# Optimization experiments

Measured on AMD Instinct MI355X. Metric: run time of the kernel, lower is better.

## Reference

```python
import jax, jax.numpy as jnp
import numpy as np

RADIUS = 0.2
NSAMPLE = 32
USE_XYZ = True


def setup_inputs() -> dict:
    key = jax.random.key(0)
    k1, k2, k3 = jax.random.split(key, 3)
    B, N, NP, C = 16, 4096, 1024, 64
    xyz = jax.random.uniform(k1, (B, N, 3), dtype=jnp.float32)
    new_xyz = jax.random.uniform(k2, (B, NP, 3), dtype=jnp.float32)
    points = jax.random.normal(k3, (B, C, N), dtype=jnp.float32)
    return {"xyz": xyz, "new_xyz": new_xyz, "points": points}


def ball_query(radius, nsample, xyz, new_xyz):
    """Replicates the CUDA ball_query: for each center, the first `nsample`
    points (in index order) with squared distance < radius^2. Unfilled slots
    are set to the first in-radius index (0 if none in radius)."""
    B, N, _ = xyz.shape
    NP = new_xyz.shape[1]
    # [B, NP, N] squared distances
    d2 = jnp.sum((new_xyz[:, :, None, :] - xyz[:, None, :, :]) ** 2, axis=-1)
    mask = d2 < (radius * radius)
    order = jnp.cumsum(mask.astype(jnp.int32), axis=-1)  # 1-based rank among in-radius pts
    cnt = order[..., -1]                                  # [B, NP] in-radius count
    # slot for each point: rank-1 if it is one of the first nsample in-radius, else dummy
    slot = jnp.where(mask & (order <= nsample), order - 1, nsample)
    bb = jnp.arange(B, dtype=jnp.int32)[:, None, None]
    pp = jnp.arange(NP, dtype=jnp.int32)[None, :, None]
    nn = jnp.broadcast_to(jnp.arange(N, dtype=jnp.int32)[None, None, :], (B, NP, N))
    idx = jnp.zeros((B, NP, nsample + 1), dtype=jnp.int32).at[bb, pp, slot].set(nn)
    idx = idx[..., :nsample]
    # replicate first in-radius index into unfilled slots (stays 0 if cnt == 0)
    filled = jnp.arange(nsample)[None, None, :] < jnp.minimum(cnt, nsample)[..., None]
    idx = jnp.where(filled, idx, idx[..., :1])
    return idx


def reference(xyz, new_xyz, points):
    idx = ball_query(RADIUS, NSAMPLE, xyz, new_xyz)          # [B, NP, NS] int32
    # gather xyz: [B, NP, NS, 3] -> [B, 3, NP, NS]
    grouped_xyz = jax.vmap(lambda x, i: x[i])(xyz, idx)
    grouped_xyz = jnp.transpose(grouped_xyz, (0, 3, 1, 2))
    # centroid subtract
    grouped_xyz = grouped_xyz - jnp.transpose(new_xyz, (0, 2, 1))[..., None]
    # gather features: points [B, C, N] -> [B, C, NP, NS]
    grouped_points = jax.vmap(lambda p, i: p[:, i])(points, idx)
    if USE_XYZ:
        new_points = jnp.concatenate([grouped_xyz, grouped_points], axis=1)
    else:
        new_points = grouped_points
    return new_points
```

## Files before the change

### kernel.cpp

```cpp
#include <hip/hip_runtime.h>
#include <hip/hip_bf16.h>

constexpr int B  = 16;
constexpr int N  = 4096;
constexpr int NP = 1024;
constexpr int C  = 64;
constexpr int NS = 32;
constexpr int OC = C + 3;
constexpr float R2 = 0.2f * 0.2f;

typedef float v4f __attribute__((ext_vector_type(4)));
typedef int   v4i __attribute__((ext_vector_type(4)));

__global__ __launch_bounds__(256)
void prep_kernel(const float* __restrict__ xyz,
                 const float* __restrict__ new_xyz,
                 const float* __restrict__ points,
                 float* __restrict__ out,
                 int* __restrict__ ws_idx,
                 float* __restrict__ pointsT)
{
    __shared__ float tile[64][65];

    if (blockIdx.x < 1024) {
        const int tb  = blockIdx.x;
        const int b   = tb >> 6;
        const int n0  = (tb & 63) << 6;
        const int col = threadIdx.x & 63;
        const int r0  = (threadIdx.x >> 6) << 4;

        const float* src = points + (size_t)b * C * N + n0;
        #pragma unroll
        for (int k = 0; k < 16; ++k) {
            const int c = r0 + k;
            tile[c][col] = src[(size_t)c * N + col];
        }
        __syncthreads();
        float* dst = pointsT + (size_t)b * N * C + (size_t)n0 * C;
        #pragma unroll
        for (int k = 0; k < 16; ++k) {
            const int n = r0 + k;
            dst[(size_t)n * C + col] = tile[col][n];
        }
        return;
    }

    const int wid  = ((blockIdx.x - 1024) << 2) + (threadIdx.x >> 6);
    const int lane = threadIdx.x & 63;
    const int b = wid >> 10;
    const int p = wid & (NP - 1);

    const float qx = new_xyz[wid * 3 + 0];
    const float qy = new_xyz[wid * 3 + 1];
    const float qz = new_xyz[wid * 3 + 2];

    const float* xb = xyz + (size_t)b * N * 3;

    float* out_x = out + (((size_t)b * OC + 0) * NP + p) * NS;
    float* out_y = out + (((size_t)b * OC + 1) * NP + p) * NS;
    float* out_z = out + (((size_t)b * OC + 2) * NP + p) * NS;
    int*   idx_p = ws_idx + (size_t)wid * NS;

    float fdx = xb[0] - qx;
    float fdy = xb[1] - qy;
    float fdz = xb[2] - qz;
    int   fidx = 0;

    int cnt = 0;
    for (int base = 0; base < N && cnt < NS; base += 128) {
        const int j0 = base + lane;
        const int j1 = base + 64 + lane;

        const float x0 = xb[j0 * 3 + 0];
        const float y0 = xb[j0 * 3 + 1];
        const float z0 = xb[j0 * 3 + 2];
        const float x1 = xb[j1 * 3 + 0];
        const float y1 = xb[j1 * 3 + 1];
        const float z1 = xb[j1 * 3 + 2];

        const float dx0 = x0 - qx, dy0 = y0 - qy, dz0 = z0 - qz;
        const float dx1 = x1 - qx, dy1 = y1 - qy, dz1 = z1 - qz;
        const float d20 = __fadd_rn(__fadd_rn(__fmul_rn(dx0, dx0),
                                              __fmul_rn(dy0, dy0)),
                                    __fmul_rn(dz0, dz0));
        const float d21 = __fadd_rn(__fadd_rn(__fmul_rn(dx1, dx1),
                                              __fmul_rn(dy1, dy1)),
                                    __fmul_rn(dz1, dz1));
        const bool in0 = d20 < R2;
        const bool in1 = d21 < R2;
        const unsigned long long m0 = __ballot(in0);
        const unsigned long long m1 = __ballot(in1);

        if (cnt == 0) {
            if (m0 != 0ull) {
                const int fl = __ffsll(m0) - 1;
                fdx = __shfl(dx0, fl, 64);
                fdy = __shfl(dy0, fl, 64);
                fdz = __shfl(dz0, fl, 64);
                fidx = base + fl;
            } else if (m1 != 0ull) {
                const int fl = __ffsll(m1) - 1;
                fdx = __shfl(dx1, fl, 64);
                fdy = __shfl(dy1, fl, 64);
                fdz = __shfl(dz1, fl, 64);
                fidx = base + 64 + fl;
            }
        }

        const unsigned long long below = (1ull << lane) - 1ull;
        if (in0) {
            const int slot = cnt + (int)__popcll(m0 & below);
            if (slot < NS) {
                idx_p[slot] = j0;
                out_x[slot] = dx0;
                out_y[slot] = dy0;
                out_z[slot] = dz0;
            }
        }
        const int c0 = cnt + (int)__popcll(m0);
        if (in1) {
            const int slot = c0 + (int)__popcll(m1 & below);
            if (slot < NS) {
                idx_p[slot] = j1;
                out_x[slot] = dx1;
                out_y[slot] = dy1;
                out_z[slot] = dz1;
            }
        }
        cnt = c0 + (int)__popcll(m1);
    }

    const int cntc = cnt < NS ? cnt : NS;
    if (lane >= cntc && lane < NS) {
        idx_p[lane] = fidx;
        out_x[lane] = fdx;
        out_y[lane] = fdy;
        out_z[lane] = fdz;
    }
}

__global__ __launch_bounds__(256)
void gather_kernel(const float* __restrict__ pointsT,
                   const int* __restrict__ ws_idx,
                   float* __restrict__ out)
{
    __shared__ float sbuf[4][NS * 65];

    const int g    = blockIdx.x;
    const int b    = g & 15;
    const int wave = threadIdx.x >> 6;
    const int lane = threadIdx.x & 63;
    const int p    = ((g >> 4) << 2) + wave;

    float* sb = &sbuf[wave][0];
    const int* idx_p = ws_idx + ((size_t)b * NP + p) * NS;
    const int myidx = (lane < NS) ? idx_p[lane] : 0;

    const float* rb = pointsT + (size_t)b * N * C;

    float vals[NS];
    #pragma unroll
    for (int s = 0; s < NS; ++s) {
        const int rn = __shfl(myidx, s, 64);
        vals[s] = rb[(size_t)rn * C + lane];
    }
    #pragma unroll
    for (int s = 0; s < NS; ++s)
        sb[s * 65 + lane] = vals[s];

    const int s    = lane & 31;
    const int half = lane >> 5;
    float* ob = out + ((size_t)b * OC + 3) * NP * NS + (size_t)p * NS;
    #pragma unroll
    for (int j = 0; j < 32; ++j) {
        const int c = 2 * j + half;
        const float v = sb[s * 65 + c];
        __builtin_nontemporal_store(v, ob + (size_t)c * NP * NS + s);
    }
}

extern "C" void kernel_launch(void* const* d_in, const int* in_sizes, int n_in,
                              void* d_out, int out_size, void* d_ws, size_t ws_size,
                              hipStream_t stream)
{
    const float* xyz     = (const float*)d_in[0];
    const float* new_xyz = (const float*)d_in[1];
    const float* points  = (const float*)d_in[2];
    float* out = (float*)d_out;

    int*   ws_idx  = (int*)d_ws;
    float* pointsT = (float*)((char*)d_ws + ((size_t)2 << 20));

    prep_kernel<<<1024 + (B * NP) / 4, 256, 0, stream>>>(
        xyz, new_xyz, points, out, ws_idx, pointsT);

    gather_kernel<<<(B * NP) / 4, 256, 0, stream>>>(pointsT, ws_idx, out);
}
```

Before: 196.8 us.

## Fuse ball query into gather kernel via LDS and vectorize output stores

Splits the transpose into its own kernel and merges the ball query with the feature gather. Indices and xyz offsets now stay in shared memory, so the idx workspace round trip goes away. The gather transposes through a padded LDS tile and writes output with 16-byte nontemporal vector stores instead of scalar stores. The cost is that query latency now sits serially inside the gather blocks, and the query no longer overlaps with the transpose blocks in a single launch.

```diff
diff --git a/kernel.cpp b/kernel.cpp
--- a/kernel.cpp
+++ b/kernel.cpp
@@ -9,46 +9,53 @@
 constexpr int OC = C + 3;
 constexpr float R2 = 0.2f * 0.2f;
 
+constexpr int TPAD = 36;
+
 typedef float v4f __attribute__((ext_vector_type(4)));
-typedef int   v4i __attribute__((ext_vector_type(4)));
 
 __global__ __launch_bounds__(256)
-void prep_kernel(const float* __restrict__ xyz,
-                 const float* __restrict__ new_xyz,
-                 const float* __restrict__ points,
-                 float* __restrict__ out,
-                 int* __restrict__ ws_idx,
-                 float* __restrict__ pointsT)
+void transpose_kernel(const float* __restrict__ points,
+                      float* __restrict__ pointsT)
 {
     __shared__ float tile[64][65];
 
-    if (blockIdx.x < 1024) {
-        const int tb  = blockIdx.x;
-        const int b   = tb >> 6;
-        const int n0  = (tb & 63) << 6;
-        const int col = threadIdx.x & 63;
-        const int r0  = (threadIdx.x >> 6) << 4;
+    const int tb  = blockIdx.x;
+    const int b   = tb >> 6;
+    const int n0  = (tb & 63) << 6;
+    const int col = threadIdx.x & 63;
+    const int r0  = (threadIdx.x >> 6) << 4;
 
-        const float* src = points + (size_t)b * C * N + n0;
-        #pragma unroll
-        for (int k = 0; k < 16; ++k) {
-            const int c = r0 + k;
-            tile[c][col] = src[(size_t)c * N + col];
-        }
-        __syncthreads();
-        float* dst = pointsT + (size_t)b * N * C + (size_t)n0 * C;
-        #pragma unroll
-        for (int k = 0; k < 16; ++k) {
-            const int n = r0 + k;
-            dst[(size_t)n * C + col] = tile[col][n];
-        }
-        return;
+    const float* src = points + (size_t)b * C * N + n0;
+    #pragma unroll
+    for (int k = 0; k < 16; ++k) {
+        const int c = r0 + k;
+        tile[c][col] = src[(size_t)c * N + col];
     }
+    __syncthreads();
+    float* dst = pointsT + (size_t)b * N * C + (size_t)n0 * C;
+    #pragma unroll
+    for (int k = 0; k < 16; ++k) {
+        const int n = r0 + k;
+        dst[(size_t)n * C + col] = tile[col][n];
+    }
+}
 
-    const int wid  = ((blockIdx.x - 1024) << 2) + (threadIdx.x >> 6);
+__global__ __launch_bounds__(256)
+void query_gather_kernel(const float* __restrict__ xyz,
+                         const float* __restrict__ new_xyz,
+                         const float* __restrict__ pointsT,
+                         float* __restrict__ out)
+{
+    __shared__ __align__(16) float sbT[4][C * TPAD];
+    __shared__ int   sidx[4][NS];
+    __shared__ float sdx[4][NS], sdy[4][NS], sdz[4][NS];
+
+    const int g    = blockIdx.x;
+    const int b    = g & 15;
+    const int wave = threadIdx.x >> 6;
     const int lane = threadIdx.x & 63;
-    const int b = wid >> 10;
-    const int p = wid & (NP - 1);
+    const int p    = ((g >> 4) << 2) + wave;
+    const int wid  = (b << 10) + p;
 
     const float qx = new_xyz[wid * 3 + 0];
     const float qy = new_xyz[wid * 3 + 1];
@@ -56,15 +63,13 @@
 
     const float* xb = xyz + (size_t)b * N * 3;
 
-    float* out_x = out + (((size_t)b * OC + 0) * NP + p) * NS;
-    float* out_y = out + (((size_t)b * OC + 1) * NP + p) * NS;
-    float* out_z = out + (((size_t)b * OC + 2) * NP + p) * NS;
-    int*   idx_p = ws_idx + (size_t)wid * NS;
-
     float fdx = xb[0] - qx;
     float fdy = xb[1] - qy;
     float fdz = xb[2] - qz;
     int   fidx = 0;
+
+    int* wi = sidx[wave];
+    float *wx = sdx[wave], *wy = sdy[wave], *wz = sdz[wave];
 
     int cnt = 0;
     for (int base = 0; base < N && cnt < NS; base += 128) {
@@ -111,20 +116,14 @@
         if (in0) {
             const int slot = cnt + (int)__popcll(m0 & below);
             if (slot < NS) {
-                idx_p[slot] = j0;
-                out_x[slot] = dx0;
-                out_y[slot] = dy0;
-                out_z[slot] = dz0;
+                wi[slot] = j0; wx[slot] = dx0; wy[slot] = dy0; wz[slot] = dz0;
             }
         }
         const int c0 = cnt + (int)__popcll(m0);
         if (in1) {
             const int slot = c0 + (int)__popcll(m1 & below);
             if (slot < NS) {
-                idx_p[slot] = j1;
-                out_x[slot] = dx1;
-                out_y[slot] = dy1;
-                out_z[slot] = dz1;
+                wi[slot] = j1; wx[slot] = dx1; wy[slot] = dy1; wz[slot] = dz1;
             }
         }
         cnt = c0 + (int)__popcll(m1);
@@ -132,50 +131,40 @@
 
     const int cntc = cnt < NS ? cnt : NS;
     if (lane >= cntc && lane < NS) {
-        idx_p[lane] = fidx;
-        out_x[lane] = fdx;
-        out_y[lane] = fdy;
-        out_z[lane] = fdz;
+        wi[lane] = fidx; wx[lane] = fdx; wy[lane] = fdy; wz[lane] = fdz;
     }
-}
 
-__global__ __launch_bounds__(256)
-void gather_kernel(const float* __restrict__ pointsT,
-                   const int* __restrict__ ws_idx,
-                   float* __restrict__ out)
-{
-    __shared__ float sbuf[4][NS * 65];
+    const size_t obase = ((size_t)b * OC) * NP * NS + (size_t)p * NS;
+    if (lane < NS) {
+        __builtin_nontemporal_store(wx[lane], out + obase + lane);
+        __builtin_nontemporal_store(wy[lane], out + obase + (size_t)NP * NS + lane);
+        __builtin_nontemporal_store(wz[lane], out + obase + (size_t)2 * NP * NS + lane);
+    }
 
-    const int g    = blockIdx.x;
-    const int b    = g & 15;
-    const int wave = threadIdx.x >> 6;
-    const int lane = threadIdx.x & 63;
-    const int p    = ((g >> 4) << 2) + wave;
+    const int myidx = wi[lane & 31];
+    const float* rb = pointsT + (size_t)b * N * C;
+    float* sT = &sbT[wave][0];
 
-    float* sb = &sbuf[wave][0];
-    const int* idx_p = ws_idx + ((size_t)b * NP + p) * NS;
-    const int myidx = (lane < NS) ? idx_p[lane] : 0;
+    #pragma unroll
+    for (int s4 = 0; s4 < 8; ++s4) {
+        v4f v;
+        #pragma unroll
+        for (int j = 0; j < 4; ++j) {
+            const int s  = (s4 << 2) + j;
+            const int rn = __shfl(myidx, s, 64);
+            v[j] = rb[(size_t)rn * C + lane];
+        }
+        *(v4f*)&sT[lane * TPAD + (s4 << 2)] = v;
+    }
 
-    const float* rb = pointsT + (size_t)b * N * C;
-
-    float vals[NS];
+    float* ob = out + obase + (size_t)3 * NP * NS;
     #pragma unroll
-    for (int s = 0; s < NS; ++s) {
-        const int rn = __shfl(myidx, s, 64);
-        vals[s] = rb[(size_t)rn * C + lane];
-    }
-    #pragma unroll
-    for (int s = 0; s < NS; ++s)
-        sb[s * 65 + lane] = vals[s];
-
-    const int s    = lane & 31;
-    const int half = lane >> 5;
-    float* ob = out + ((size_t)b * OC + 3) * NP * NS + (size_t)p * NS;
-    #pragma unroll
-    for (int j = 0; j < 32; ++j) {
-        const int c = 2 * j + half;
-        const float v = sb[s * 65 + c];
-        __builtin_nontemporal_store(v, ob + (size_t)c * NP * NS + s);
+    for (int k = 0; k < 8; ++k) {
+        const int q  = (k << 6) + lane;
+        const int c  = q >> 3;
+        const int s4 = q & 7;
+        const v4f v = *(const v4f*)&sT[c * TPAD + (s4 << 2)];
+        __builtin_nontemporal_store(v, (v4f*)(ob + (size_t)c * NP * NS + (s4 << 2)));
     }
 }
 
@@ -188,11 +177,10 @@
     const float* points  = (const float*)d_in[2];
     float* out = (float*)d_out;
 
-    int*   ws_idx  = (int*)d_ws;
-    float* pointsT = (float*)((char*)d_ws + ((size_t)2 << 20));
+    float* pointsT = (float*)d_ws;
 
-    prep_kernel<<<1024 + (B * NP) / 4, 256, 0, stream>>>(
-        xyz, new_xyz, points, out, ws_idx, pointsT);
+    transpose_kernel<<<B * (N / 64), 256, 0, stream>>>(points, pointsT);
 
-    gather_kernel<<<(B * NP) / 4, 256, 0, stream>>>(pointsT, ws_idx, out);
+    query_gather_kernel<<<(B * NP) / 4, 256, 0, stream>>>(
+        xyz, new_xyz, pointsT, out);
 }
```

After: 196.0 us. No clear change (-0.4%).
